# Kernel optimization log

Hardware: AMD Instinct MI355X
Metric: run time of the kernel (lower is better)

## Reference

```python
import jax, jax.numpy as jnp
import numpy as np

NUM_POSES = 200
N = 1048576

def _exp_vector(w):
    # Rodrigues formula: so(3) vector [N,3] -> rotation matrix [N,3,3]
    theta2 = jnp.sum(w * w, axis=-1)                     # [N]
    theta = jnp.sqrt(theta2 + 1e-12)                     # safe norm
    a = (jnp.sin(theta) / theta)[:, None, None]          # sin(t)/t
    b = ((1.0 - jnp.cos(theta)) / theta2.clip(1e-12))[:, None, None]
    wx, wy, wz = w[:, 0], w[:, 1], w[:, 2]
    zero = jnp.zeros_like(wx)
    K = jnp.stack([
        jnp.stack([zero, -wz, wy], axis=-1),
        jnp.stack([wz, zero, -wx], axis=-1),
        jnp.stack([-wy, wx, zero], axis=-1),
    ], axis=-2)                                          # [N,3,3] skew
    I = jnp.eye(3, dtype=w.dtype)
    return I + a * K + b * jnp.einsum('nij,njk->nik', K, K)

def setup_inputs() -> dict:
    key = jax.random.key(0)
    k1, k2, k3, k4 = jax.random.split(key, 4)
    n = jax.random.randint(k1, (N,), 0, NUM_POSES, dtype=jnp.int64)
    E = jax.random.normal(k2, (N, 4, 4), dtype=jnp.float32)
    R = jax.random.normal(k3, (NUM_POSES, 3), dtype=jnp.float32) * 0.1
    T = jax.random.normal(k4, (NUM_POSES, 3), dtype=jnp.float32) * 0.1
    return {"n": n, "E": E, "R": R, "T": T}

def reference(n, E, R, T):
    # mode == 'camera': pose = n
    Rg = R[n]                                            # [N,3] gather
    Tg = T[n]                                            # [N,3]
    rot = _exp_vector(Rg)                                # [N,3,3]
    top = jnp.concatenate([rot, Tg[:, :, None]], axis=2) # [N,3,4]
    bottom = jnp.broadcast_to(
        jnp.array([[0., 0., 0., 1.]], dtype=E.dtype)[None], (n.shape[0], 1, 4))
    M = jnp.concatenate([top, bottom], axis=1)           # [N,4,4]
    return jnp.einsum('nij,njk->nik', M, E)
```

## Files before the change

kernel.cpp:

```cpp
#include <hip/hip_runtime.h>

#define NUM_POSES 200

typedef float        v4f __attribute__((ext_vector_type(4)));
typedef unsigned int v2u __attribute__((ext_vector_type(2)));

__device__ __forceinline__ float bf2f(unsigned int u16) {
    union { unsigned int u; float f; } v; v.u = u16 << 16; return v.f;
}
__device__ __forceinline__ unsigned int f2bf(float f) {
    union { float f; unsigned int u; } v; v.f = f;
    unsigned int r = v.u + 0x7FFFu + ((v.u >> 16) & 1u);
    return r >> 16;
}

__global__ void prep_kernel(const unsigned short* __restrict__ E16,
                            const unsigned int* __restrict__ n32,
                            const void* __restrict__ Rv,
                            const void* __restrict__ Tv,
                            int* __restrict__ flags,
                            float* __restrict__ M) {
    __shared__ unsigned int sany;
    int t = threadIdx.x;
    if (t == 0) sany = 0u;
    __syncthreads();
    unsigned int local = 0u;
    for (int k = t; k < 4096; k += 256) {
        float a = fabsf(bf2f(E16[k]));
        if (!(a <= 1e6f)) local |= 1u;
    }
    if (n32[2 * t + 1] != 0u) local |= 2u;
    if (local) atomicOr(&sany, local);
    __syncthreads();
    unsigned int s = sany;
    if (t == 0) {
        flags[0] = (s & 1u) ? 1 : 0;
        flags[1] = (s & 2u) ? 1 : 0;
    }
    if (t >= NUM_POSES) return;
    int p = t;
    float wx, wy, wz, tx, ty, tz;
    if (s & 1u) {
        const float* R = (const float*)Rv; const float* T = (const float*)Tv;
        wx = R[3*p+0]; wy = R[3*p+1]; wz = R[3*p+2];
        tx = T[3*p+0]; ty = T[3*p+1]; tz = T[3*p+2];
    } else {
        const unsigned short* R = (const unsigned short*)Rv;
        const unsigned short* T = (const unsigned short*)Tv;
        wx = bf2f(R[3*p+0]); wy = bf2f(R[3*p+1]); wz = bf2f(R[3*p+2]);
        tx = bf2f(T[3*p+0]); ty = bf2f(T[3*p+1]); tz = bf2f(T[3*p+2]);
    }
    float t2 = wx*wx + wy*wy + wz*wz;
    float th = sqrtf(t2 + 1e-12f);
    float a  = sinf(th) / th;
    float b  = (1.0f - cosf(th)) / fmaxf(t2, 1e-12f);

    float* m = M + p * 16;
    m[0]  = 1.0f - b * (wy*wy + wz*wz);
    m[1]  = -a * wz + b * wx * wy;
    m[2]  =  a * wy + b * wx * wz;
    m[3]  = tx;
    m[4]  =  a * wz + b * wx * wy;
    m[5]  = 1.0f - b * (wx*wx + wz*wz);
    m[6]  = -a * wx + b * wy * wz;
    m[7]  = ty;
    m[8]  = -a * wy + b * wx * wz;
    m[9]  =  a * wx + b * wy * wz;
    m[10] = 1.0f - b * (wx*wx + wy*wy);
    m[11] = tz;
    m[12] = 0.0f; m[13] = 0.0f; m[14] = 0.0f; m[15] = 1.0f;
}

__global__ __launch_bounds__(256) void apply_kernel(
        const void* __restrict__ nin,
        const void* __restrict__ Ein,
        const float4* __restrict__ M,
        void* __restrict__ outv,
        const int* __restrict__ flags,
        int N) {
    int t = blockIdx.x * blockDim.x + threadIdx.x;
    int e = t >> 2;
    int r = t & 3;
    if (e >= N) return;
    const int e_is_f32 = flags[0];
    const int n_is_i32 = flags[1];

    long long p = n_is_i32 ? (long long)((const int*)nin)[e]
                           : ((const long long*)nin)[e];
    float4 m = M[p * 4 + r];

    if (e_is_f32) {
        const v4f* Ee = (const v4f*)Ein + 4 * (size_t)e;
        v4f E0 = __builtin_nontemporal_load(Ee + 0);
        v4f E1 = __builtin_nontemporal_load(Ee + 1);
        v4f E2 = __builtin_nontemporal_load(Ee + 2);
        v4f E3 = __builtin_nontemporal_load(Ee + 3);
        v4f o;
        o.x = m.x*E0.x + m.y*E1.x + m.z*E2.x + m.w*E3.x;
        o.y = m.x*E0.y + m.y*E1.y + m.z*E2.y + m.w*E3.y;
        o.z = m.x*E0.z + m.y*E1.z + m.z*E2.z + m.w*E3.z;
        o.w = m.x*E0.w + m.y*E1.w + m.z*E2.w + m.w*E3.w;
        __builtin_nontemporal_store(o, (v4f*)outv + t);
    } else {
        const v2u* Ee = (const v2u*)Ein + 4 * (size_t)e;
        v2u w0 = __builtin_nontemporal_load(Ee + 0);
        v2u w1 = __builtin_nontemporal_load(Ee + 1);
        v2u w2 = __builtin_nontemporal_load(Ee + 2);
        v2u w3 = __builtin_nontemporal_load(Ee + 3);
        float E0x = bf2f(w0.x & 0xFFFFu), E0y = bf2f(w0.x >> 16), E0z = bf2f(w0.y & 0xFFFFu), E0w = bf2f(w0.y >> 16);
        float E1x = bf2f(w1.x & 0xFFFFu), E1y = bf2f(w1.x >> 16), E1z = bf2f(w1.y & 0xFFFFu), E1w = bf2f(w1.y >> 16);
        float E2x = bf2f(w2.x & 0xFFFFu), E2y = bf2f(w2.x >> 16), E2z = bf2f(w2.y & 0xFFFFu), E2w = bf2f(w2.y >> 16);
        float E3x = bf2f(w3.x & 0xFFFFu), E3y = bf2f(w3.x >> 16), E3z = bf2f(w3.y & 0xFFFFu), E3w = bf2f(w3.y >> 16);
        float ox = m.x*E0x + m.y*E1x + m.z*E2x + m.w*E3x;
        float oy = m.x*E0y + m.y*E1y + m.z*E2y + m.w*E3y;
        float oz = m.x*E0z + m.y*E1z + m.z*E2z + m.w*E3z;
        float ow = m.x*E0w + m.y*E1w + m.z*E2w + m.w*E3w;
        v2u pk;
        pk.x = f2bf(ox) | (f2bf(oy) << 16);
        pk.y = f2bf(oz) | (f2bf(ow) << 16);
        __builtin_nontemporal_store(pk, (v2u*)outv + t);
    }
}

extern "C" void kernel_launch(void* const* d_in, const int* in_sizes, int n_in,
                              void* d_out, int out_size, void* d_ws, size_t ws_size,
                              hipStream_t stream) {
    const void* n = d_in[0];
    const void* E = d_in[1];
    const void* R = d_in[2];
    const void* T = d_in[3];
    int*    flags = (int*)d_ws;
    float*      M = (float*)((char*)d_ws + 256);
    const int   N = in_sizes[0];

    prep_kernel<<<1, 256, 0, stream>>>((const unsigned short*)E,
                                       (const unsigned int*)n, R, T, flags, M);
    const int rows = N * 4;
    apply_kernel<<<(rows + 255) / 256, 256, 0, stream>>>(
        n, E, (const float4*)M, d_out, flags, N);
}
```

Baseline: 145.8 us.

## Load one E row per lane and share rows via DPP quad rotations

Each lane now loads only its own row of E instead of all four rows, and gets the other three rows of the 4x4 from neighbouring lanes with DPP quad-permute moves. The per-pose matrix is stored pre-rotated so the coefficients line up with the rotated rows. The cost targeted is the fourfold redundant global/cache traffic on E. Each thread also handles two rows spaced a grid-stride apart, which halves the block count. The risk is extra cross-lane moves and the early return inside the unrolled loop, although all four lanes of a quad still exit together.

Result: faster. 134.5 us (-7.7%).

```diff
diff --git a/kernel.cpp b/kernel.cpp
--- a/kernel.cpp
+++ b/kernel.cpp
@@ -13,6 +13,23 @@
     unsigned int r = v.u + 0x7FFFu + ((v.u >> 16) & 1u);
     return r >> 16;
 }
+
+template <int CTRL>
+__device__ __forceinline__ float rotf(float v) {
+    int i = __builtin_bit_cast(int, v);
+    i = __builtin_amdgcn_mov_dpp(i, CTRL, 0xF, 0xF, true);
+    return __builtin_bit_cast(float, i);
+}
+template <int CTRL>
+__device__ __forceinline__ v4f rot4(v4f v) {
+    v4f r;
+    r.x = rotf<CTRL>(v.x); r.y = rotf<CTRL>(v.y);
+    r.z = rotf<CTRL>(v.z); r.w = rotf<CTRL>(v.w);
+    return r;
+}
+#define ROT1 0x39
+#define ROT2 0x4E
+#define ROT3 0x93
 
 __global__ void prep_kernel(const unsigned short* __restrict__ E16,
                             const unsigned int* __restrict__ n32,
@@ -33,10 +50,7 @@
     if (local) atomicOr(&sany, local);
     __syncthreads();
     unsigned int s = sany;
-    if (t == 0) {
-        flags[0] = (s & 1u) ? 1 : 0;
-        flags[1] = (s & 2u) ? 1 : 0;
-    }
+    if (t == 0) { flags[0] = (s & 1u) ? 1 : 0; flags[1] = (s & 2u) ? 1 : 0; }
     if (t >= NUM_POSES) return;
     int p = t;
     float wx, wy, wz, tx, ty, tz;
@@ -55,70 +69,73 @@
     float a  = sinf(th) / th;
     float b  = (1.0f - cosf(th)) / fmaxf(t2, 1e-12f);
 
-    float* m = M + p * 16;
-    m[0]  = 1.0f - b * (wy*wy + wz*wz);
-    m[1]  = -a * wz + b * wx * wy;
-    m[2]  =  a * wy + b * wx * wz;
-    m[3]  = tx;
-    m[4]  =  a * wz + b * wx * wy;
-    m[5]  = 1.0f - b * (wx*wx + wz*wz);
-    m[6]  = -a * wx + b * wy * wz;
-    m[7]  = ty;
-    m[8]  = -a * wy + b * wx * wz;
-    m[9]  =  a * wx + b * wy * wz;
-    m[10] = 1.0f - b * (wx*wx + wy*wy);
-    m[11] = tz;
-    m[12] = 0.0f; m[13] = 0.0f; m[14] = 0.0f; m[15] = 1.0f;
+    float mm[4][4];
+    mm[0][0] = 1.0f - b * (wy*wy + wz*wz);
+    mm[0][1] = -a * wz + b * wx * wy;
+    mm[0][2] =  a * wy + b * wx * wz;
+    mm[0][3] = tx;
+    mm[1][0] =  a * wz + b * wx * wy;
+    mm[1][1] = 1.0f - b * (wx*wx + wz*wz);
+    mm[1][2] = -a * wx + b * wy * wz;
+    mm[1][3] = ty;
+    mm[2][0] = -a * wy + b * wx * wz;
+    mm[2][1] =  a * wx + b * wy * wz;
+    mm[2][2] = 1.0f - b * (wx*wx + wy*wy);
+    mm[2][3] = tz;
+    mm[3][0] = 0.0f; mm[3][1] = 0.0f; mm[3][2] = 0.0f; mm[3][3] = 1.0f;
+    float* mo = M + p * 16;
+    #pragma unroll
+    for (int r = 0; r < 4; ++r)
+        #pragma unroll
+        for (int k = 0; k < 4; ++k)
+            mo[r*4 + k] = mm[r][(r + k) & 3];
 }
 
 __global__ __launch_bounds__(256) void apply_kernel(
         const void* __restrict__ nin,
         const void* __restrict__ Ein,
-        const float4* __restrict__ M,
+        const float4* __restrict__ Mrot,
         void* __restrict__ outv,
         const int* __restrict__ flags,
         int N) {
-    int t = blockIdx.x * blockDim.x + threadIdx.x;
-    int e = t >> 2;
-    int r = t & 3;
-    if (e >= N) return;
+    const int TOT  = gridDim.x * blockDim.x;
+    const int rows = N * 4;
+    int t0 = blockIdx.x * blockDim.x + threadIdx.x;
+    int t1 = t0 + TOT;
     const int e_is_f32 = flags[0];
     const int n_is_i32 = flags[1];
 
-    long long p = n_is_i32 ? (long long)((const int*)nin)[e]
-                           : ((const long long*)nin)[e];
-    float4 m = M[p * 4 + r];
+    #pragma unroll
+    for (int u = 0; u < 2; ++u) {
+        int t = u ? t1 : t0;
+        if (t >= rows) return;
+        int e = t >> 2;
+        int r = t & 3;
+        long long p = n_is_i32 ? (long long)((const int*)nin)[e]
+                               : ((const long long*)nin)[e];
+        float4 c = Mrot[p * 4 + r];
 
-    if (e_is_f32) {
-        const v4f* Ee = (const v4f*)Ein + 4 * (size_t)e;
-        v4f E0 = __builtin_nontemporal_load(Ee + 0);
-        v4f E1 = __builtin_nontemporal_load(Ee + 1);
-        v4f E2 = __builtin_nontemporal_load(Ee + 2);
-        v4f E3 = __builtin_nontemporal_load(Ee + 3);
-        v4f o;
-        o.x = m.x*E0.x + m.y*E1.x + m.z*E2.x + m.w*E3.x;
-        o.y = m.x*E0.y + m.y*E1.y + m.z*E2.y + m.w*E3.y;
-        o.z = m.x*E0.z + m.y*E1.z + m.z*E2.z + m.w*E3.z;
-        o.w = m.x*E0.w + m.y*E1.w + m.z*E2.w + m.w*E3.w;
-        __builtin_nontemporal_store(o, (v4f*)outv + t);
-    } else {
-        const v2u* Ee = (const v2u*)Ein + 4 * (size_t)e;
-        v2u w0 = __builtin_nontemporal_load(Ee + 0);
-        v2u w1 = __builtin_nontemporal_load(Ee + 1);
-        v2u w2 = __builtin_nontemporal_load(Ee + 2);
-        v2u w3 = __builtin_nontemporal_load(Ee + 3);
-        float E0x = bf2f(w0.x & 0xFFFFu), E0y = bf2f(w0.x >> 16), E0z = bf2f(w0.y & 0xFFFFu), E0w = bf2f(w0.y >> 16);
-        float E1x = bf2f(w1.x & 0xFFFFu), E1y = bf2f(w1.x >> 16), E1z = bf2f(w1.y & 0xFFFFu), E1w = bf2f(w1.y >> 16);
-        float E2x = bf2f(w2.x & 0xFFFFu), E2y = bf2f(w2.x >> 16), E2z = bf2f(w2.y & 0xFFFFu), E2w = bf2f(w2.y >> 16);
-        float E3x = bf2f(w3.x & 0xFFFFu), E3y = bf2f(w3.x >> 16), E3z = bf2f(w3.y & 0xFFFFu), E3w = bf2f(w3.y >> 16);
-        float ox = m.x*E0x + m.y*E1x + m.z*E2x + m.w*E3x;
-        float oy = m.x*E0y + m.y*E1y + m.z*E2y + m.w*E3y;
-        float oz = m.x*E0z + m.y*E1z + m.z*E2z + m.w*E3z;
-        float ow = m.x*E0w + m.y*E1w + m.z*E2w + m.w*E3w;
-        v2u pk;
-        pk.x = f2bf(ox) | (f2bf(oy) << 16);
-        pk.y = f2bf(oz) | (f2bf(ow) << 16);
-        __builtin_nontemporal_store(pk, (v2u*)outv + t);
+        if (e_is_f32) {
+            v4f self = __builtin_nontemporal_load((const v4f*)Ein + t);
+            v4f e1 = rot4<ROT1>(self);
+            v4f e2 = rot4<ROT2>(self);
+            v4f e3 = rot4<ROT3>(self);
+            v4f o = c.x * self + c.y * e1 + c.z * e2 + c.w * e3;
+            __builtin_nontemporal_store(o, (v4f*)outv + t);
+        } else {
+            v2u raw = __builtin_nontemporal_load((const v2u*)Ein + t);
+            v4f self;
+            self.x = bf2f(raw.x & 0xFFFFu); self.y = bf2f(raw.x >> 16);
+            self.z = bf2f(raw.y & 0xFFFFu); self.w = bf2f(raw.y >> 16);
+            v4f e1 = rot4<ROT1>(self);
+            v4f e2 = rot4<ROT2>(self);
+            v4f e3 = rot4<ROT3>(self);
+            v4f o = c.x * self + c.y * e1 + c.z * e2 + c.w * e3;
+            v2u pk;
+            pk.x = f2bf(o.x) | (f2bf(o.y) << 16);
+            pk.y = f2bf(o.z) | (f2bf(o.w) << 16);
+            __builtin_nontemporal_store(pk, (v2u*)outv + t);
+        }
     }
 }
 
@@ -135,7 +152,8 @@
 
     prep_kernel<<<1, 256, 0, stream>>>((const unsigned short*)E,
                                        (const unsigned int*)n, R, T, flags, M);
-    const int rows = N * 4;
-    apply_kernel<<<(rows + 255) / 256, 256, 0, stream>>>(
+    const int rows   = N * 4;
+    const int blocks = (rows + 511) / 512;
+    apply_kernel<<<blocks, 256, 0, stream>>>(
         n, E, (const float4*)M, d_out, flags, N);
 }
```
